# Optimization experiments

Hardware: AMD Instinct MI355X
Metric: run time of the kernel (lower is better)

The kernel has to match this reference:

```python
import jax, jax.numpy as jnp
import numpy as np

S, N, H = 1024, 64, 1024  # source len, batch, hidden_size
INPUT_SIZE = 1024         # attention projection dim (linear1/linear2 out)


def setup_inputs() -> dict:
    key = jax.random.key(0)
    ks = jax.random.split(key, 8)
    sc_h = 1.0 / np.sqrt(H)
    sc_i = 1.0 / np.sqrt(INPUT_SIZE)
    return {
        "out_e": jax.random.normal(ks[0], (S, N, H), dtype=jnp.float32),
        "hidden_d": jax.random.normal(ks[1], (1, N, H), dtype=jnp.float32),
        # torch Linear weights are [out_features, in_features]
        "W1": jax.random.uniform(ks[2], (INPUT_SIZE, H), jnp.float32, -sc_h, sc_h),
        "b1": jax.random.uniform(ks[3], (INPUT_SIZE,), jnp.float32, -sc_h, sc_h),
        "W2": jax.random.uniform(ks[4], (INPUT_SIZE, H), jnp.float32, -sc_h, sc_h),
        "b2": jax.random.uniform(ks[5], (INPUT_SIZE,), jnp.float32, -sc_h, sc_h),
        "W3": jax.random.uniform(ks[6], (1, INPUT_SIZE), jnp.float32, -sc_i, sc_i),
        "b3": jax.random.uniform(ks[7], (1,), jnp.float32, -sc_i, sc_i),
    }


def reference(out_e, hidden_d, W1, b1, W2, b2, W3, b3):
    # hidden_d [1,N,H] broadcast to [S,N,H] (torch .repeat)
    s = out_e.shape[0]
    hd = jnp.broadcast_to(hidden_d, (s,) + hidden_d.shape[1:])
    # a: [S,N,1] = linear3(tanh(linear1(hd) + linear2(out_e)))
    e = jnp.tanh(hd @ W1.T + b1 + out_e @ W2.T + b2)
    a = e @ W3.T + b3
    # softmax over the source dim (dim=0 in torch)
    alpha = jax.nn.softmax(a, axis=0)          # [S,N,1]
    c = jnp.einsum('sne,snh->enh', alpha, out_e)  # [1,N,H]
    return (c, alpha)
```

## Files before the change

kernel.cpp:

```cpp
#include <hip/hip_runtime.h>
#include <hip/hip_fp16.h>

#define S_LEN 1024
#define N_B   64
#define H_DIM 1024
#define I_DIM 1024
#define M_ROWS (S_LEN * N_B)

typedef __attribute__((ext_vector_type(8))) _Float16 half8;
typedef __attribute__((ext_vector_type(4))) _Float16 half4;
typedef __attribute__((ext_vector_type(4))) float    f32x4;

__device__ __forceinline__ void gload16(const void* g, void* l) {
  __builtin_amdgcn_global_load_lds(
      (const __attribute__((address_space(1))) unsigned int*)g,
      (__attribute__((address_space(3))) unsigned int*)l, 16, 0, 0);
}

__global__ void cvt_f32_f16(const float* __restrict__ src,
                            _Float16* __restrict__ dst, int n4) {
  int idx = blockIdx.x * blockDim.x + threadIdx.x;
  int stride = gridDim.x * blockDim.x;
  const float4* s4 = (const float4*)src;
  half4* d4 = (half4*)dst;
  for (int i = idx; i < n4; i += stride) {
    float4 v = s4[i];
    half4 h;
    h[0] = (_Float16)v.x; h[1] = (_Float16)v.y;
    h[2] = (_Float16)v.z; h[3] = (_Float16)v.w;
    d4[i] = h;
  }
}

__global__ void u1_kernel(const float* __restrict__ hd,
                          const float* __restrict__ W1,
                          const float* __restrict__ b1,
                          const float* __restrict__ b2,
                          float* __restrict__ u1) {
  __shared__ float hs[4 * 1024];
  int nb = blockIdx.x & 15;
  int ib = blockIdx.x >> 4;
  int t = threadIdx.x;
  int n0 = nb * 4;

  const float4* g4 = (const float4*)(hd + (size_t)n0 * 1024);
  float4* h4 = (float4*)hs;
#pragma unroll
  for (int r = 0; r < 4; ++r) h4[r * 256 + t] = g4[r * 256 + t];
  __syncthreads();

  int il = t >> 2, q = t & 3;
  int i = ib * 64 + il;
  const float4* w4 = (const float4*)(W1 + (size_t)i * 1024 + q * 256);
  float s0 = 0.f, s1 = 0.f, s2 = 0.f, s3 = 0.f;
  for (int hh = 0; hh < 64; ++hh) {
    float4 wv = w4[hh];
    int hb = q * 256 + hh * 4;
    float4 v0 = *(const float4*)&hs[0 * 1024 + hb];
    float4 v1 = *(const float4*)&hs[1 * 1024 + hb];
    float4 v2 = *(const float4*)&hs[2 * 1024 + hb];
    float4 v3 = *(const float4*)&hs[3 * 1024 + hb];
    s0 += wv.x * v0.x + wv.y * v0.y + wv.z * v0.z + wv.w * v0.w;
    s1 += wv.x * v1.x + wv.y * v1.y + wv.z * v1.z + wv.w * v1.w;
    s2 += wv.x * v2.x + wv.y * v2.y + wv.z * v2.z + wv.w * v2.w;
    s3 += wv.x * v3.x + wv.y * v3.y + wv.z * v3.z + wv.w * v3.w;
  }
  s0 += __shfl_xor(s0, 1); s0 += __shfl_xor(s0, 2);
  s1 += __shfl_xor(s1, 1); s1 += __shfl_xor(s1, 2);
  s2 += __shfl_xor(s2, 1); s2 += __shfl_xor(s2, 2);
  s3 += __shfl_xor(s3, 1); s3 += __shfl_xor(s3, 2);
  if (q == 0) {
    float bb = b1[i] + b2[i];
    u1[(size_t)(n0 + 0) * 1024 + i] = s0 + bb;
    u1[(size_t)(n0 + 1) * 1024 + i] = s1 + bb;
    u1[(size_t)(n0 + 2) * 1024 + i] = s2 + bb;
    u1[(size_t)(n0 + 3) * 1024 + i] = s3 + bb;
  }
}

__global__ __launch_bounds__(256) void fused_gemm_tanh(
    const _Float16* __restrict__ A,
    const _Float16* __restrict__ B,
    const float* __restrict__ u1,
    const float* __restrict__ W3,
    float* __restrict__ a_ws)
{
  __shared__ __align__(16) _Float16 As[2][128 * 32];
  __shared__ __align__(16) _Float16 Bs[2][128 * 32];

  const int t = threadIdx.x;
  const int lane = t & 63;
  const int w = t >> 6;
  const int wr = w >> 1, wc = w & 1;
  const int bx = blockIdx.x;
  const int xcd = bx & 7;
  const int j = bx >> 3;
  const int rb = xcd + ((j >> 3) << 3);
  const int cb = j & 7;
  const int m0 = rb * 128, i0 = cb * 128;

  const int strow = t >> 2;
  const int stcol = (t & 3) * 8;
  const _Float16* gA = A + (size_t)(m0 + strow) * 1024 + stcol;
  const _Float16* gB = B + (size_t)(i0 + strow) * 1024 + stcol;
  const int ldsoff = strow * 32 + stcol;

  f32x4 acc[4][4] = {};

  gload16(gA,             &As[0][ldsoff]);
  gload16(gA + 64 * 1024, &As[0][ldsoff + 64 * 32]);
  gload16(gB,             &Bs[0][ldsoff]);
  gload16(gB + 64 * 1024, &Bs[0][ldsoff + 64 * 32]);
  __syncthreads();

  const int fr = lane & 15;
  const int kg = lane >> 4;
  const int aoff = (wr * 64 + fr) * 32 + kg * 8;
  const int boff = (wc * 64 + fr) * 32 + kg * 8;

  for (int kt = 0; kt < 32; ++kt) {
    const int buf = kt & 1;
    if (kt < 31) {
      const _Float16* gA2 = gA + (kt + 1) * 32;
      const _Float16* gB2 = gB + (kt + 1) * 32;
      gload16(gA2,             &As[buf ^ 1][ldsoff]);
      gload16(gA2 + 64 * 1024, &As[buf ^ 1][ldsoff + 64 * 32]);
      gload16(gB2,             &Bs[buf ^ 1][ldsoff]);
      gload16(gB2 + 64 * 1024, &Bs[buf ^ 1][ldsoff + 64 * 32]);
    }
    half8 af[4], bf[4];
#pragma unroll
    for (int mi = 0; mi < 4; ++mi)
      af[mi] = *(const half8*)&As[buf][aoff + mi * 16 * 32];
#pragma unroll
    for (int ni = 0; ni < 4; ++ni)
      bf[ni] = *(const half8*)&Bs[buf][boff + ni * 16 * 32];
#pragma unroll
    for (int mi = 0; mi < 4; ++mi)
#pragma unroll
      for (int ni = 0; ni < 4; ++ni)
        acc[mi][ni] = __builtin_amdgcn_mfma_f32_16x16x32_f16(
            af[mi], bf[ni], acc[mi][ni], 0, 0, 0);
    __syncthreads();
  }

  float w3v[4];
#pragma unroll
  for (int ni = 0; ni < 4; ++ni)
    w3v[ni] = W3[i0 + wc * 64 + ni * 16 + fr];

#pragma unroll
  for (int mi = 0; mi < 4; ++mi) {
#pragma unroll
    for (int jj = 0; jj < 4; ++jj) {
      int m = m0 + wr * 64 + mi * 16 + kg * 4 + jj;
      int n = m & 63;
      const float* u1row = u1 + (size_t)n * 1024 + i0 + wc * 64;
      float s = 0.f;
#pragma unroll
      for (int ni = 0; ni < 4; ++ni) {
        float e = acc[mi][ni][jj] + u1row[ni * 16 + fr];
        float th = 1.f - 2.f / (__expf(2.f * e) + 1.f);
        s += th * w3v[ni];
      }
      s += __shfl_xor(s, 1);
      s += __shfl_xor(s, 2);
      s += __shfl_xor(s, 4);
      s += __shfl_xor(s, 8);
      if (fr == 0) atomicAdd(&a_ws[m], s);
    }
  }
}

__global__ void softmax_col(const float* __restrict__ a_ws,
                            float* __restrict__ alpha) {
  int n = blockIdx.x;
  int t = threadIdx.x;
  __shared__ float red[256];
  float v[4];
  float mx = -1e30f;
#pragma unroll
  for (int q = 0; q < 4; ++q) {
    v[q] = a_ws[(size_t)(t + q * 256) * 64 + n];
    mx = fmaxf(mx, v[q]);
  }
  red[t] = mx; __syncthreads();
  for (int off = 128; off > 0; off >>= 1) {
    if (t < off) red[t] = fmaxf(red[t], red[t + off]);
    __syncthreads();
  }
  mx = red[0];
  __syncthreads();
  float sum = 0.f;
#pragma unroll
  for (int q = 0; q < 4; ++q) { v[q] = __expf(v[q] - mx); sum += v[q]; }
  red[t] = sum; __syncthreads();
  for (int off = 128; off > 0; off >>= 1) {
    if (t < off) red[t] += red[t + off];
    __syncthreads();
  }
  float inv = 1.f / red[0];
#pragma unroll
  for (int q = 0; q < 4; ++q)
    alpha[(size_t)(t + q * 256) * 64 + n] = v[q] * inv;
}

__global__ void weighted_sum(const _Float16* __restrict__ oe,
                             const float* __restrict__ alpha,
                             float* __restrict__ cout) {
  int n = blockIdx.x & 63;
  int sc = blockIdx.x >> 6;
  int t = threadIdx.x;
  __shared__ float al[64];
  if (t < 64) al[t] = alpha[(size_t)(sc * 64 + t) * 64 + n];
  __syncthreads();
  float a0 = 0.f, a1 = 0.f, a2 = 0.f, a3 = 0.f;
#pragma unroll 4
  for (int sl = 0; sl < 64; ++sl) {
    float a = al[sl];
    int s = sc * 64 + sl;
    half4 x = *(const half4*)(oe + (size_t)(s * 64 + n) * 1024 + t * 4);
    a0 += a * (float)x[0]; a1 += a * (float)x[1];
    a2 += a * (float)x[2]; a3 += a * (float)x[3];
  }
  float* c = cout + (size_t)n * 1024 + t * 4;
  atomicAdd(c + 0, a0);
  atomicAdd(c + 1, a1);
  atomicAdd(c + 2, a2);
  atomicAdd(c + 3, a3);
}

extern "C" void kernel_launch(void* const* d_in, const int* in_sizes, int n_in,
                              void* d_out, int out_size, void* d_ws,
                              size_t ws_size, hipStream_t stream) {
  const float* out_e    = (const float*)d_in[0];
  const float* hidden_d = (const float*)d_in[1];
  const float* W1       = (const float*)d_in[2];
  const float* b1       = (const float*)d_in[3];
  const float* W2       = (const float*)d_in[4];
  const float* b2       = (const float*)d_in[5];
  const float* W3       = (const float*)d_in[6];

  char* ws = (char*)d_ws;
  _Float16* oe16 = (_Float16*)ws;
  _Float16* w216 = (_Float16*)(ws + 134217728);
  float* u1   = (float*)(ws + 134217728 + 2097152);
  float* a_ws = (float*)(ws + 134217728 + 2097152 + 262144);

  float* c_out = (float*)d_out;
  float* alpha = (float*)d_out + 65536;

  hipLaunchKernelGGL(cvt_f32_f16, dim3(2048), dim3(256), 0, stream,
                     out_e, oe16, 67108864 / 4);
  hipLaunchKernelGGL(cvt_f32_f16, dim3(256), dim3(256), 0, stream,
                     W2, w216, 1048576 / 4);
  hipLaunchKernelGGL(u1_kernel, dim3(256), dim3(256), 0, stream,
                     hidden_d, W1, b1, b2, u1);
  hipMemsetAsync(a_ws, 0, 65536 * 4, stream);
  hipMemsetAsync(c_out, 0, 65536 * 4, stream);
  hipLaunchKernelGGL(fused_gemm_tanh, dim3(4096), dim3(256), 0, stream,
                     oe16, w216, u1, W3, a_ws);
  hipLaunchKernelGGL(softmax_col, dim3(64), dim3(256), 0, stream,
                     a_ws, alpha);
  hipLaunchKernelGGL(weighted_sum, dim3(1024), dim3(256), 0, stream,
                     oe16, alpha, c_out);
}
```

Before: 655.0 us.

## Swizzle GEMM LDS layout, widen fp16 conversion, fold memsets into kernels

The GEMM staging now applies an XOR swizzle to the 16-byte chunk index in the LDS tiles, and the fragment reads use the matching swizzle, to cut LDS bank conflicts on the half8 operand loads. The fp32-to-fp16 conversion kernel now handles eight elements per thread with 16-byte stores and twice as many blocks. The two hipMemsetAsync calls are removed: u1_kernel zeroes a_ws and softmax_col zeroes c_out, which saves two stream operations but places extra writes inside those kernels.

```diff
diff --git a/kernel.cpp b/kernel.cpp
--- a/kernel.cpp
+++ b/kernel.cpp
@@ -5,7 +5,6 @@
 #define N_B   64
 #define H_DIM 1024
 #define I_DIM 1024
-#define M_ROWS (S_LEN * N_B)
 
 typedef __attribute__((ext_vector_type(8))) _Float16 half8;
 typedef __attribute__((ext_vector_type(4))) _Float16 half4;
@@ -18,17 +17,19 @@
 }
 
 __global__ void cvt_f32_f16(const float* __restrict__ src,
-                            _Float16* __restrict__ dst, int n4) {
+                            _Float16* __restrict__ dst, int n8) {
   int idx = blockIdx.x * blockDim.x + threadIdx.x;
   int stride = gridDim.x * blockDim.x;
   const float4* s4 = (const float4*)src;
-  half4* d4 = (half4*)dst;
-  for (int i = idx; i < n4; i += stride) {
-    float4 v = s4[i];
-    half4 h;
-    h[0] = (_Float16)v.x; h[1] = (_Float16)v.y;
-    h[2] = (_Float16)v.z; h[3] = (_Float16)v.w;
-    d4[i] = h;
+  half8* d8 = (half8*)dst;
+  for (int i = idx; i < n8; i += stride) {
+    float4 a = s4[2 * i], b = s4[2 * i + 1];
+    half8 h;
+    h[0] = (_Float16)a.x; h[1] = (_Float16)a.y;
+    h[2] = (_Float16)a.z; h[3] = (_Float16)a.w;
+    h[4] = (_Float16)b.x; h[5] = (_Float16)b.y;
+    h[6] = (_Float16)b.z; h[7] = (_Float16)b.w;
+    d8[i] = h;
   }
 }
 
@@ -36,12 +37,15 @@
                           const float* __restrict__ W1,
                           const float* __restrict__ b1,
                           const float* __restrict__ b2,
-                          float* __restrict__ u1) {
+                          float* __restrict__ u1,
+                          float* __restrict__ a_ws) {
   __shared__ float hs[4 * 1024];
   int nb = blockIdx.x & 15;
   int ib = blockIdx.x >> 4;
   int t = threadIdx.x;
   int n0 = nb * 4;
+
+  a_ws[blockIdx.x * 256 + t] = 0.f;
 
   const float4* g4 = (const float4*)(hd + (size_t)n0 * 1024);
   float4* h4 = (float4*)hs;
@@ -100,10 +104,10 @@
   const int m0 = rb * 128, i0 = cb * 128;
 
   const int strow = t >> 2;
-  const int stcol = (t & 3) * 8;
+  const int stcol = ((t & 3) ^ ((t >> 2) & 3)) * 8;
   const _Float16* gA = A + (size_t)(m0 + strow) * 1024 + stcol;
   const _Float16* gB = B + (size_t)(i0 + strow) * 1024 + stcol;
-  const int ldsoff = strow * 32 + stcol;
+  const int ldsoff = strow * 32 + (t & 3) * 8;
 
   f32x4 acc[4][4] = {};
 
@@ -115,8 +119,9 @@
 
   const int fr = lane & 15;
   const int kg = lane >> 4;
-  const int aoff = (wr * 64 + fr) * 32 + kg * 8;
-  const int boff = (wc * 64 + fr) * 32 + kg * 8;
+  const int un = (kg ^ (fr & 3)) * 8;
+  const int aoff = (wr * 64 + fr) * 32 + un;
+  const int boff = (wc * 64 + fr) * 32 + un;
 
   for (int kt = 0; kt < 32; ++kt) {
     const int buf = kt & 1;
@@ -173,10 +178,13 @@
 }
 
 __global__ void softmax_col(const float* __restrict__ a_ws,
-                            float* __restrict__ alpha) {
+                            float* __restrict__ alpha,
+                            float* __restrict__ c_out) {
   int n = blockIdx.x;
   int t = threadIdx.x;
   __shared__ float red[256];
+#pragma unroll
+  for (int q = 0; q < 4; ++q) c_out[(size_t)n * 1024 + q * 256 + t] = 0.f;
   float v[4];
   float mx = -1e30f;
 #pragma unroll
@@ -250,18 +258,16 @@
   float* c_out = (float*)d_out;
   float* alpha = (float*)d_out + 65536;
 
-  hipLaunchKernelGGL(cvt_f32_f16, dim3(2048), dim3(256), 0, stream,
-                     out_e, oe16, 67108864 / 4);
-  hipLaunchKernelGGL(cvt_f32_f16, dim3(256), dim3(256), 0, stream,
-                     W2, w216, 1048576 / 4);
+  hipLaunchKernelGGL(cvt_f32_f16, dim3(4096), dim3(256), 0, stream,
+                     out_e, oe16, 67108864 / 8);
+  hipLaunchKernelGGL(cvt_f32_f16, dim3(512), dim3(256), 0, stream,
+                     W2, w216, 1048576 / 8);
   hipLaunchKernelGGL(u1_kernel, dim3(256), dim3(256), 0, stream,
-                     hidden_d, W1, b1, b2, u1);
-  hipMemsetAsync(a_ws, 0, 65536 * 4, stream);
-  hipMemsetAsync(c_out, 0, 65536 * 4, stream);
+                     hidden_d, W1, b1, b2, u1, a_ws);
   hipLaunchKernelGGL(fused_gemm_tanh, dim3(4096), dim3(256), 0, stream,
                      oe16, w216, u1, W3, a_ws);
   hipLaunchKernelGGL(softmax_col, dim3(64), dim3(256), 0, stream,
-                     a_ws, alpha);
+                     a_ws, alpha, c_out);
   hipLaunchKernelGGL(weighted_sum, dim3(1024), dim3(256), 0, stream,
                      oe16, alpha, c_out);
 }
```

After: 666.4 us. No clear change (+1.7%).
